# Kernel tuning notes

Measured on AMD Instinct MI355X. Metric: run time of the kernel, lower is better.

Reference implementation:

```python
import jax, jax.numpy as jnp
import numpy as np

IN_FEATURES = 2048
OUT_FEATURES = 4096
NUM_SHIFTS = 10  # perms


def setup_inputs() -> dict:
    key = jax.random.key(0)
    kx, kw = jax.random.split(key)
    x = jax.random.normal(kx, (4, 2048, IN_FEATURES), dtype=jnp.float32)
    # nn.Linear weight: (out_features, in_features), Kaiming-uniform-ish init
    bound = 1.0 / np.sqrt(IN_FEATURES)
    W = jax.random.uniform(kw, (OUT_FEATURES, IN_FEATURES), dtype=jnp.float32,
                           minval=-bound, maxval=bound)
    return {"x": x, "W": W}


def _combined_weight(W):
    # Wt: (in, out). Sum of all weight variants; sum_i(x @ W_i) == x @ sum_i(W_i).
    Wt = W.T
    Weff = Wt + jnp.flip(Wt, axis=0) + jnp.flip(Wt, axis=1)
    for i in range(NUM_SHIFTS // 2):
        Weff = Weff + jnp.roll(Wt, shift=i + 1, axis=1)
        Weff = Weff + jnp.roll(Wt, shift=i + 1, axis=0)
    return Weff  # (in, out)


def reference(x, W):
    # reg_out (x @ W.T) + flipped + rolled variants, collapsed into one GEMM
    Weff = _combined_weight(W)
    return jnp.einsum('bsi,io->bso', x, Weff)
```

## Files before the change

kernel.cpp:

```cpp
#include <hip/hip_runtime.h>
#include <hip/hip_bf16.h>
#include <stdint.h>

#define M_DIM 8192
#define K_DIM 2048
#define N_DIM 4096
#define BM 256
#define BN 256
#define BK 64
#define NT (K_DIM / BK)
#define NITER (NT / 2)

typedef __attribute__((ext_vector_type(8))) short bf16x8;
typedef __attribute__((ext_vector_type(4))) float f32x4;

__device__ __forceinline__ unsigned short f2bfu(float f) {
    __hip_bfloat16 h = __float2bfloat16(f);
    return __builtin_bit_cast(unsigned short, h);
}

__global__ void build_weff(const float* __restrict__ W, unsigned short* __restrict__ WT) {
    const int o = blockIdx.x;
    const float* wo  = W + (size_t)o * K_DIM;
    const float* wfo = W + (size_t)(N_DIM - 1 - o) * K_DIM;
    const float* wr0 = W + (size_t)((o - 1) & (N_DIM - 1)) * K_DIM;
    const float* wr1 = W + (size_t)((o - 2) & (N_DIM - 1)) * K_DIM;
    const float* wr2 = W + (size_t)((o - 3) & (N_DIM - 1)) * K_DIM;
    const float* wr3 = W + (size_t)((o - 4) & (N_DIM - 1)) * K_DIM;
    const float* wr4 = W + (size_t)((o - 5) & (N_DIM - 1)) * K_DIM;
    for (int i = threadIdx.x; i < K_DIM; i += 256) {
        float acc = wo[i] + wo[K_DIM - 1 - i] + wfo[i];
        acc += wo[(i - 1) & (K_DIM - 1)];
        acc += wo[(i - 2) & (K_DIM - 1)];
        acc += wo[(i - 3) & (K_DIM - 1)];
        acc += wo[(i - 4) & (K_DIM - 1)];
        acc += wo[(i - 5) & (K_DIM - 1)];
        acc += wr0[i] + wr1[i] + wr2[i] + wr3[i] + wr4[i];
        WT[(size_t)o * K_DIM + i] = f2bfu(acc);
    }
}

__global__ void cvt_x_kernel(const float* __restrict__ x, unsigned short* __restrict__ xb) {
    const int idx = blockIdx.x * 256 + threadIdx.x;
    float4 v = ((const float4*)x)[idx];
    ushort4 o;
    o.x = f2bfu(v.x); o.y = f2bfu(v.y); o.z = f2bfu(v.z); o.w = f2bfu(v.w);
    ((ushort4*)xb)[idx] = o;
}

__global__ __launch_bounds__(512, 2) void gemm8p(const unsigned short* __restrict__ Ab,
                                                 const unsigned short* __restrict__ Bt,
                                                 float* __restrict__ C) {
    __shared__ __align__(16) char smem[2 * 65536];

    const int tid  = threadIdx.x;
    const int wave = tid >> 6;
    const int lane = tid & 63;

    const int nwg = gridDim.x;
    const int cpx = nwg >> 3;
    const int wg  = (blockIdx.x & 7) * cpx + (blockIdx.x >> 3);
    const int nbn = N_DIM / BN;
    const int bm0 = (wg / nbn) * BM;
    const int bn0 = (wg % nbn) * BN;

    const int wr = wave >> 2;
    const int wc = wave & 3;

    const int srow = tid >> 3;
    const int lsw  = (lane & 7) ^ ((lane >> 3) & 7);
    const unsigned short* gA0 = Ab + (size_t)(bm0 + srow) * K_DIM + lsw * 8;
    const unsigned short* gB0 = Bt + (size_t)(bn0 + srow) * K_DIM + lsw * 8;

    const int r16  = lane & 15;
    const int x7   = lane & 7;
    const int ksl0 = (((lane >> 4)    ) ^ x7) * 16;
    const int ksl1 = (((lane >> 4) | 4) ^ x7) * 16;
    const int aRow = (wr * 128 + r16) * 128;
    const int bRow = (wc * 64  + r16) * 128 + 32768;

    f32x4  acc[8][4] = {};
    bf16x8 b[4][2];

#define STAGE_HALF(gbase, opoff, h, t, p) do {                                              \
    char* lds_ = smem + (p) * 65536 + (opoff) + (h) * 16384 + wave * 1024;                  \
    const unsigned short* g_ = (gbase) + (size_t)((h) * 128) * K_DIM + (t) * BK;            \
    __builtin_amdgcn_global_load_lds(                                                        \
        (const __attribute__((address_space(1))) unsigned int*)g_,                           \
        (__attribute__((address_space(3))) unsigned int*)lds_, 16, 0, 0);                    \
    __builtin_amdgcn_global_load_lds(                                                        \
        (const __attribute__((address_space(1))) unsigned int*)(g_ + (size_t)64 * K_DIM),    \
        (__attribute__((address_space(3))) unsigned int*)(lds_ + 8192), 16, 0, 0);           \
} while (0)

#define PHASE(P, Q, LOADB, STAGE_STMT, VM_STMT) do {                                        \
    const char* base_ = smem + (P) * 65536;                                                 \
    bf16x8 a_[2][2];                                                                        \
    if (LOADB) {                                                                            \
        _Pragma("unroll")                                                                   \
        for (int fn = 0; fn < 4; ++fn) {                                                    \
            b[fn][0] = *(const bf16x8*)(base_ + bRow + fn * 2048 + ksl0);                   \
            b[fn][1] = *(const bf16x8*)(base_ + bRow + fn * 2048 + ksl1);                   \
        }                                                                                   \
    }                                                                                       \
    a_[0][0] = *(const bf16x8*)(base_ + aRow + (Q) * 4096 + ksl0);                          \
    a_[0][1] = *(const bf16x8*)(base_ + aRow + (Q) * 4096 + ksl1);                          \
    a_[1][0] = *(const bf16x8*)(base_ + aRow + (Q) * 4096 + 2048 + ksl0);                   \
    a_[1][1] = *(const bf16x8*)(base_ + aRow + (Q) * 4096 + 2048 + ksl1);                   \
    STAGE_STMT;                                                                             \
    __builtin_amdgcn_s_barrier();                                                           \
    asm volatile("s_waitcnt lgkmcnt(0)" ::: "memory");                                      \
    __builtin_amdgcn_sched_barrier(0);                                                      \
    __builtin_amdgcn_s_setprio(1);                                                          \
    _Pragma("unroll")                                                                       \
    for (int fm = 0; fm < 2; ++fm)                                                          \
        _Pragma("unroll")                                                                   \
        for (int fn = 0; fn < 4; ++fn) {                                                    \
            acc[(Q)*2 + fm][fn] = __builtin_amdgcn_mfma_f32_16x16x32_bf16(                  \
                a_[fm][0], b[fn][0], acc[(Q)*2 + fm][fn], 0, 0, 0);                         \
            acc[(Q)*2 + fm][fn] = __builtin_amdgcn_mfma_f32_16x16x32_bf16(                  \
                a_[fm][1], b[fn][1], acc[(Q)*2 + fm][fn], 0, 0, 0);                         \
        }                                                                                   \
    __builtin_amdgcn_s_setprio(0);                                                          \
    VM_STMT;                                                                                \
    __builtin_amdgcn_s_barrier();                                                           \
} while (0)

    STAGE_HALF(gA0, 0,     0, 0, 0);
    STAGE_HALF(gA0, 0,     1, 0, 0);
    STAGE_HALF(gB0, 32768, 0, 0, 0);
    STAGE_HALF(gB0, 32768, 1, 0, 0);
    STAGE_HALF(gB0, 32768, 0, 1, 1);
    STAGE_HALF(gB0, 32768, 1, 1, 1);
    asm volatile("s_waitcnt vmcnt(4)" ::: "memory");
    __builtin_amdgcn_s_barrier();

    for (int u = 0; u < NITER; ++u) {
        const bool last = (u == NITER - 1);
        const int  t1 = 2 * u + 1, t2 = 2 * u + 2, t3 = 2 * u + 3;

        PHASE(0, 0, 1, { STAGE_HALF(gA0, 0, 0, t1, 1); }, {});
        PHASE(0, 1, 0, { STAGE_HALF(gA0, 0, 1, t1, 1); }, {});
        PHASE(0, 2, 0, { if (!last) STAGE_HALF(gB0, 32768, 0, t2, 0); }, {});
        PHASE(0, 3, 0, { if (!last) STAGE_HALF(gB0, 32768, 1, t2, 0); },
              { if (last) asm volatile("s_waitcnt vmcnt(0)" ::: "memory");
                else      asm volatile("s_waitcnt vmcnt(4)" ::: "memory"); });
        PHASE(1, 0, 1, { if (!last) STAGE_HALF(gA0, 0, 0, t2, 0); }, {});
        PHASE(1, 1, 0, { if (!last) STAGE_HALF(gA0, 0, 1, t2, 0); }, {});
        PHASE(1, 2, 0, { if (!last) STAGE_HALF(gB0, 32768, 0, t3, 1); }, {});
        PHASE(1, 3, 0, { if (!last) STAGE_HALF(gB0, 32768, 1, t3, 1); },
              { if (!last) asm volatile("s_waitcnt vmcnt(4)" ::: "memory"); });
    }
#undef PHASE
#undef STAGE_HALF

    const int crow = (lane >> 4) * 4;
    const int ccol = lane & 15;
    float* Cb = C + (size_t)(bm0 + wr * 128 + crow) * N_DIM + (bn0 + wc * 64 + ccol);
#pragma unroll
    for (int fm = 0; fm < 8; ++fm)
#pragma unroll
        for (int fn = 0; fn < 4; ++fn)
#pragma unroll
            for (int r = 0; r < 4; ++r)
                Cb[(size_t)(fm * 16 + r) * N_DIM + fn * 16] = acc[fm][fn][r];
}

extern "C" void kernel_launch(void* const* d_in, const int* in_sizes, int n_in,
                              void* d_out, int out_size, void* d_ws, size_t ws_size,
                              hipStream_t stream) {
    const float* x = (const float*)d_in[0];
    const float* W = (const float*)d_in[1];
    float* out = (float*)d_out;

    unsigned short* xb = (unsigned short*)d_ws;
    unsigned short* wt = (unsigned short*)((char*)d_ws + (size_t)M_DIM * K_DIM * 2);

    build_weff<<<N_DIM, 256, 0, stream>>>(W, wt);
    cvt_x_kernel<<<(M_DIM * K_DIM) / 4 / 256, 256, 0, stream>>>(x, xb);

    dim3 grid((M_DIM / BM) * (N_DIM / BN));
    gemm8p<<<grid, 512, 0, stream>>>(xb, wt, out);
}
```

Baseline: 179.9 us.

## Switch GEMM to 32x32x16 MFMA tiles and stage weight row in LDS

The GEMM inner loop moves from 16x16x32 bf16 MFMAs to 32x32x16 MFMAs, with new LDS fragment addressing, accumulator layout and epilogue store mapping. This cuts the number of MFMA issues and LDS reads per k-step. The weight-combination kernel now stages the row being processed in shared memory so its shifted and flipped reads hit LDS rather than global memory. The output store pattern changes to match the 32x32 accumulator layout, which carries a risk of indexing errors.

```diff
diff --git a/kernel.cpp b/kernel.cpp
--- a/kernel.cpp
+++ b/kernel.cpp
@@ -11,32 +11,41 @@
 #define NT (K_DIM / BK)
 #define NITER (NT / 2)
 
-typedef __attribute__((ext_vector_type(8))) short bf16x8;
-typedef __attribute__((ext_vector_type(4))) float f32x4;
+typedef __attribute__((ext_vector_type(8)))  short bf16x8;
+typedef __attribute__((ext_vector_type(16))) float f32x16;
 
 __device__ __forceinline__ unsigned short f2bfu(float f) {
     __hip_bfloat16 h = __float2bfloat16(f);
     return __builtin_bit_cast(unsigned short, h);
 }
 
-__global__ void build_weff(const float* __restrict__ W, unsigned short* __restrict__ WT) {
+__global__ __launch_bounds__(256) void build_weff(const float* __restrict__ W,
+                                                  unsigned short* __restrict__ WT) {
+    __shared__ float row[K_DIM];
     const int o = blockIdx.x;
-    const float* wo  = W + (size_t)o * K_DIM;
-    const float* wfo = W + (size_t)(N_DIM - 1 - o) * K_DIM;
-    const float* wr0 = W + (size_t)((o - 1) & (N_DIM - 1)) * K_DIM;
-    const float* wr1 = W + (size_t)((o - 2) & (N_DIM - 1)) * K_DIM;
-    const float* wr2 = W + (size_t)((o - 3) & (N_DIM - 1)) * K_DIM;
-    const float* wr3 = W + (size_t)((o - 4) & (N_DIM - 1)) * K_DIM;
-    const float* wr4 = W + (size_t)((o - 5) & (N_DIM - 1)) * K_DIM;
-    for (int i = threadIdx.x; i < K_DIM; i += 256) {
-        float acc = wo[i] + wo[K_DIM - 1 - i] + wfo[i];
-        acc += wo[(i - 1) & (K_DIM - 1)];
-        acc += wo[(i - 2) & (K_DIM - 1)];
-        acc += wo[(i - 3) & (K_DIM - 1)];
-        acc += wo[(i - 4) & (K_DIM - 1)];
-        acc += wo[(i - 5) & (K_DIM - 1)];
-        acc += wr0[i] + wr1[i] + wr2[i] + wr3[i] + wr4[i];
-        WT[(size_t)o * K_DIM + i] = f2bfu(acc);
+    const float* wo = W + (size_t)o * K_DIM;
+#pragma unroll
+    for (int t = 0; t < 2; ++t)
+        ((float4*)row)[threadIdx.x + 256 * t] = ((const float4*)wo)[threadIdx.x + 256 * t];
+    __syncthreads();
+
+    const float* rF = W + (size_t)(N_DIM - 1 - o) * K_DIM;
+    const float* r1 = W + (size_t)((o - 1) & (N_DIM - 1)) * K_DIM;
+    const float* r2 = W + (size_t)((o - 2) & (N_DIM - 1)) * K_DIM;
+    const float* r3 = W + (size_t)((o - 3) & (N_DIM - 1)) * K_DIM;
+    const float* r4 = W + (size_t)((o - 4) & (N_DIM - 1)) * K_DIM;
+    const float* r5 = W + (size_t)((o - 5) & (N_DIM - 1)) * K_DIM;
+
+    unsigned short* wt = WT + (size_t)o * K_DIM;
+#pragma unroll
+    for (int j = 0; j < 8; ++j) {
+        const int i = threadIdx.x + 256 * j;
+        float s = row[i] + row[K_DIM - 1 - i]
+                + row[(i - 1) & (K_DIM - 1)] + row[(i - 2) & (K_DIM - 1)]
+                + row[(i - 3) & (K_DIM - 1)] + row[(i - 4) & (K_DIM - 1)]
+                + row[(i - 5) & (K_DIM - 1)];
+        s += rF[i] + r1[i] + r2[i] + r3[i] + r4[i] + r5[i];
+        wt[i] = f2bfu(s);
     }
 }
 
@@ -72,15 +81,18 @@
     const unsigned short* gA0 = Ab + (size_t)(bm0 + srow) * K_DIM + lsw * 8;
     const unsigned short* gB0 = Bt + (size_t)(bn0 + srow) * K_DIM + lsw * 8;
 
-    const int r16  = lane & 15;
-    const int x7   = lane & 7;
-    const int ksl0 = (((lane >> 4)    ) ^ x7) * 16;
-    const int ksl1 = (((lane >> 4) | 4) ^ x7) * 16;
-    const int aRow = (wr * 128 + r16) * 128;
-    const int bRow = (wc * 64  + r16) * 128 + 32768;
+    const int l31 = lane & 31;
+    const int x7  = lane & 7;
+    const int kh  = lane >> 5;
+    int sl[4];
+#pragma unroll
+    for (int ks = 0; ks < 4; ++ks) sl[ks] = ((kh + 2 * ks) ^ x7) * 16;
+    const int aRow = (wr * 128 + l31) * 128;
+    const int bR0  = (wc * 64 + l31) * 128 + 32768;
+    const int bR1  = bR0 + 32 * 128;
 
-    f32x4  acc[8][4] = {};
-    bf16x8 b[4][2];
+    f32x16 acc[8] = {};
+    bf16x8 b[2][4];
 
 #define STAGE_HALF(gbase, opoff, h, t, p) do {                                              \
     char* lds_ = smem + (p) * 65536 + (opoff) + (h) * 16384 + wave * 1024;                  \
@@ -95,32 +107,29 @@
 
 #define PHASE(P, Q, LOADB, STAGE_STMT, VM_STMT) do {                                        \
     const char* base_ = smem + (P) * 65536;                                                 \
-    bf16x8 a_[2][2];                                                                        \
+    bf16x8 a_[4];                                                                           \
     if (LOADB) {                                                                            \
         _Pragma("unroll")                                                                   \
-        for (int fn = 0; fn < 4; ++fn) {                                                    \
-            b[fn][0] = *(const bf16x8*)(base_ + bRow + fn * 2048 + ksl0);                   \
-            b[fn][1] = *(const bf16x8*)(base_ + bRow + fn * 2048 + ksl1);                   \
+        for (int ks = 0; ks < 4; ++ks) {                                                    \
+            b[0][ks] = *(const bf16x8*)(base_ + bR0 + sl[ks]);                              \
+            b[1][ks] = *(const bf16x8*)(base_ + bR1 + sl[ks]);                              \
         }                                                                                   \
     }                                                                                       \
-    a_[0][0] = *(const bf16x8*)(base_ + aRow + (Q) * 4096 + ksl0);                          \
-    a_[0][1] = *(const bf16x8*)(base_ + aRow + (Q) * 4096 + ksl1);                          \
-    a_[1][0] = *(const bf16x8*)(base_ + aRow + (Q) * 4096 + 2048 + ksl0);                   \
-    a_[1][1] = *(const bf16x8*)(base_ + aRow + (Q) * 4096 + 2048 + ksl1);                   \
+    _Pragma("unroll")                                                                       \
+    for (int ks = 0; ks < 4; ++ks)                                                          \
+        a_[ks] = *(const bf16x8*)(base_ + aRow + (Q) * 4096 + sl[ks]);                      \
     STAGE_STMT;                                                                             \
     __builtin_amdgcn_s_barrier();                                                           \
     asm volatile("s_waitcnt lgkmcnt(0)" ::: "memory");                                      \
     __builtin_amdgcn_sched_barrier(0);                                                      \
     __builtin_amdgcn_s_setprio(1);                                                          \
     _Pragma("unroll")                                                                       \
-    for (int fm = 0; fm < 2; ++fm)                                                          \
-        _Pragma("unroll")                                                                   \
-        for (int fn = 0; fn < 4; ++fn) {                                                    \
-            acc[(Q)*2 + fm][fn] = __builtin_amdgcn_mfma_f32_16x16x32_bf16(                  \
-                a_[fm][0], b[fn][0], acc[(Q)*2 + fm][fn], 0, 0, 0);                         \
-            acc[(Q)*2 + fm][fn] = __builtin_amdgcn_mfma_f32_16x16x32_bf16(                  \
-                a_[fm][1], b[fn][1], acc[(Q)*2 + fm][fn], 0, 0, 0);                         \
-        }                                                                                   \
+    for (int ks = 0; ks < 4; ++ks) {                                                        \
+        acc[(Q) * 2 + 0] = __builtin_amdgcn_mfma_f32_32x32x16_bf16(                         \
+            a_[ks], b[0][ks], acc[(Q) * 2 + 0], 0, 0, 0);                                   \
+        acc[(Q) * 2 + 1] = __builtin_amdgcn_mfma_f32_32x32x16_bf16(                         \
+            a_[ks], b[1][ks], acc[(Q) * 2 + 1], 0, 0, 0);                                   \
+    }                                                                                       \
     __builtin_amdgcn_s_setprio(0);                                                          \
     VM_STMT;                                                                                \
     __builtin_amdgcn_s_barrier();                                                           \
@@ -154,16 +163,17 @@
 #undef PHASE
 #undef STAGE_HALF
 
-    const int crow = (lane >> 4) * 4;
-    const int ccol = lane & 15;
-    float* Cb = C + (size_t)(bm0 + wr * 128 + crow) * N_DIM + (bn0 + wc * 64 + ccol);
+    const int rb = (lane >> 5) * 4;
+    float* Cb = C + (size_t)(bm0 + wr * 128) * N_DIM + (bn0 + wc * 64 + l31);
 #pragma unroll
-    for (int fm = 0; fm < 8; ++fm)
+    for (int mf = 0; mf < 4; ++mf)
 #pragma unroll
-        for (int fn = 0; fn < 4; ++fn)
+        for (int nf = 0; nf < 2; ++nf)
 #pragma unroll
-            for (int r = 0; r < 4; ++r)
-                Cb[(size_t)(fm * 16 + r) * N_DIM + fn * 16] = acc[fm][fn][r];
+            for (int r = 0; r < 16; ++r) {
+                const int rr = mf * 32 + (r & 3) + 8 * (r >> 2) + rb;
+                Cb[(size_t)rr * N_DIM + nf * 32] = acc[mf * 2 + nf][r];
+            }
 }
 
 extern "C" void kernel_launch(void* const* d_in, const int* in_sizes, int n_in,
```

New measurement: 188.9 us. +5.0%, slower.
